# Performance work log

Hardware: AMD Instinct MI355X
Metric: run time of the kernel (lower is better)

Reference implementation:

```python
import jax, jax.numpy as jnp
import numpy as np

LN_EPS = 1e-5


def setup_inputs() -> dict:
    key = jax.random.key(0)
    ks = jax.random.split(key, 5)
    N, E, D = 50000, 600000, 128
    x = jax.random.normal(ks[0], (N, D), dtype=jnp.float32)
    edge_index = jax.random.randint(ks[1], (2, E), 0, N, dtype=jnp.int64)
    W_l = jax.random.normal(ks[2], (D, D), dtype=jnp.float32) * (1.0 / np.sqrt(D))
    b_l = jnp.zeros((D,), dtype=jnp.float32)
    W_r = jax.random.normal(ks[3], (D, D), dtype=jnp.float32) * (1.0 / np.sqrt(D))
    gamma = jnp.ones((D,), dtype=jnp.float32)
    beta = jnp.zeros((D,), dtype=jnp.float32)
    return {"x": x, "edge_index": edge_index, "W_l": W_l, "b_l": b_l,
            "W_r": W_r, "gamma": gamma, "beta": beta}


def reference(x, edge_index, W_l, b_l, W_r, gamma, beta):
    # SAGEConv (mean aggregation): out = lin_l(mean_{j in N(i)} x_j) + lin_r(x_i)
    N = x.shape[0]
    src, dst = edge_index[0], edge_index[1]
    msg = x[src]                                                # (E, D) gather
    agg = jax.ops.segment_sum(msg, dst, num_segments=N)         # (N, D) scatter-add
    cnt = jax.ops.segment_sum(jnp.ones_like(dst, dtype=x.dtype), dst, num_segments=N)
    mean = agg / jnp.maximum(cnt, 1.0)[:, None]
    h = mean @ W_l.T + b_l + x @ W_r.T                          # (N, D)
    # LayerNorm over feature dim
    mu = jnp.mean(h, axis=-1, keepdims=True)
    var = jnp.mean(jnp.square(h - mu), axis=-1, keepdims=True)
    h = (h - mu) * jax.lax.rsqrt(var + LN_EPS) * gamma + beta
    # ReLU; Dropout is identity in eval mode
    return jax.nn.relu(h)
```

## Files before the change

kernel.cpp:

```cpp
#include <hip/hip_runtime.h>
#include <stdint.h>

#define DIM 128
#define LN_EPS 1e-5f
#define BROWS 32
#define BINB 128
#define SCAP 16
#define NBKT_MAX 1600
#define LELLS 56
#define LOVF 64
#define OVFCAP 4096
#define ATS 264
#define PINIT ((int)0xAAAAAAAA)

typedef __attribute__((ext_vector_type(8))) short bf16x8;
typedef __attribute__((ext_vector_type(4))) float f32x4;

static __device__ __forceinline__ uint16_t f2bf(float f) {
    uint32_t u = __float_as_uint(f);
    return (uint16_t)((u + 0x7fffu + ((u >> 16) & 1u)) >> 16);
}
static __device__ __forceinline__ float bf_lo(uint32_t w) {
    return __uint_as_float(w << 16);
}
static __device__ __forceinline__ float bf_hi(uint32_t w) {
    return __uint_as_float(w & 0xffff0000u);
}

__global__ __launch_bounds__(256) void bin_kernel(
    const int* __restrict__ ei,
    const float* __restrict__ x,
    const float* __restrict__ Wl,
    const float* __restrict__ Wr,
    int* __restrict__ cnt, uint32_t* __restrict__ bedge,
    int* __restrict__ novf, int* __restrict__ ovf,
    uint16_t* __restrict__ x16, uint16_t* __restrict__ wc,
    int E, int N, int nbkt)
{
    __shared__ int hist[NBKT_MAX];
    const int t = threadIdx.x, b = blockIdx.x;

    for (int i = t; i < nbkt; i += 256) hist[i] = 0;
    __syncthreads();

    const int chunk = (E + BINB - 1) / BINB;
    const int e0 = b * chunk;
    const int e1 = (e0 + chunk < E) ? e0 + chunk : E;

    for (int e = e0 + t; e < e1; e += 256)
        atomicAdd(&hist[ei[E + e] >> 5], 1);
    __syncthreads();

    for (int i = t; i < nbkt; i += 256) {
        cnt[(size_t)i * BINB + b] = hist[i];
        hist[i] = 0;
    }
    __syncthreads();

    for (int e = e0 + t; e < e1; e += 256) {
        int src = ei[e];
        int dst = ei[E + e];
        int bkt = dst >> 5;
        int r = atomicAdd(&hist[bkt], 1);
        if (r < SCAP) {
            bedge[((size_t)bkt * BINB + b) * SCAP + r] =
                ((uint32_t)(dst & 31) << 27) | (uint32_t)src;
        } else {
            int q = atomicAdd(novf, 1) - PINIT;
            if (q >= 0 && q < OVFCAP) { ovf[2 * q] = dst; ovf[2 * q + 1] = src; }
        }
    }

    {
        int tid = b * 256 + t, nth = BINB * 256;
        int nxp = (N * DIM) >> 1;
        for (int i = tid; i < nxp; i += nth) {
            float2 v = *(const float2*)(x + 2 * i);
            uint32_t u = ((uint32_t)f2bf(v.y) << 16) | (uint32_t)f2bf(v.x);
            ((uint32_t*)x16)[i] = u;
        }
        for (int i = tid; i < DIM * 256; i += nth) {
            int d = i >> 8, k = i & 255;
            float v = (k < DIM) ? Wl[d * DIM + k] : Wr[d * DIM + (k - DIM)];
            wc[i] = f2bf(v);
        }
    }
}

__global__ __launch_bounds__(256, 4) void fused_kernel(
    const uint16_t* __restrict__ x16,
    const int* __restrict__ cnt,
    const uint32_t* __restrict__ bedge,
    const int* __restrict__ novf,
    const int* __restrict__ ovf,
    const uint16_t* __restrict__ wc,
    const float* __restrict__ bl,
    const float* __restrict__ gma,
    const float* __restrict__ bta,
    float* __restrict__ out,
    int N, int E)
{
    __shared__ int ell_s[BROWS][LELLS];
    __shared__ int cnt_s[BROWS];
    __shared__ int lovf_s[LOVF];
    __shared__ int nlovf_s;
    __shared__ uint16_t atile[2][16 * ATS];
    __shared__ float pln[2][16][2][2];

    const int t    = threadIdx.x;
    const int lane = t & 63;
    const int w    = t >> 6;
    const int p    = w >> 1;
    const int h    = w & 1;
    const int tile_row0 = blockIdx.x * BROWS + p * 16;
    const int grow0     = tile_row0 + h * 8;
    const int lb        = p * 16 + h * 8;

    if (t < BROWS) cnt_s[t] = 0;
    if (t == BROWS) nlovf_s = 0;
    __syncthreads();

    if (t < BINB) {
        int c = cnt[(size_t)blockIdx.x * BINB + t];
        c = (c < SCAP) ? c : SCAP;
        const uint32_t* sp = bedge + ((size_t)blockIdx.x * BINB + t) * SCAP;
        for (int r = 0; r < c; ++r) {
            uint32_t pk = sp[r];
            int local = pk >> 27;
            int rr = atomicAdd(&cnt_s[local], 1);
            if (rr < LELLS) ell_s[local][rr] = (int)(pk & 0x07FFFFFF);
            else {
                int q = atomicAdd(&nlovf_s, 1);
                if (q < LOVF) lovf_s[q] = (int)pk;
            }
        }
    }
    __syncthreads();

    int dgx[8], nell[8], mx = 0;
    #pragma unroll
    for (int r = 0; r < 8; ++r) {
        int d = __builtin_amdgcn_readfirstlane(cnt_s[lb + r]);
        dgx[r] = d;
        int tt = d < LELLS ? d : LELLS;
        nell[r] = tt;
        mx = (tt > mx) ? tt : mx;
    }

    int sidx[8];
    #pragma unroll
    for (int r = 0; r < 8; ++r)
        sidx[r] = (lane < nell[r]) ? ell_s[lb + r][lane] : 0;

    float m0[8], m1[8];
    #pragma unroll
    for (int r = 0; r < 8; ++r) { m0[r] = 0.0f; m1[r] = 0.0f; }

    for (int j = 0; j < mx; ++j) {
        #pragma unroll
        for (int r = 0; r < 8; ++r) {
            float pr = (j < nell[r]) ? 1.0f : 0.0f;
            int s = __builtin_amdgcn_readlane(sidx[r], j);
            uint32_t u = *(const uint32_t*)(x16 + (size_t)s * DIM + 2 * lane);
            m0[r] = fmaf(pr, bf_lo(u), m0[r]);
            m1[r] = fmaf(pr, bf_hi(u), m1[r]);
        }
    }

    {
        int nl = __builtin_amdgcn_readfirstlane(nlovf_s);
        nl = (nl < 0) ? 0 : (nl > LOVF ? LOVF : nl);
        for (int i = 0; i < nl; ++i) {
            uint32_t pk = (uint32_t)lovf_s[i];
            int local = pk >> 27;
            if (local >= lb && local < lb + 8) {
                int srco = (int)(pk & 0x07FFFFFF);
                uint32_t u = *(const uint32_t*)(x16 + (size_t)srco * DIM + 2 * lane);
                float v0 = bf_lo(u), v1 = bf_hi(u);
                #pragma unroll
                for (int r = 0; r < 8; ++r) {
                    float pr = (local == lb + r) ? 1.0f : 0.0f;
                    m0[r] = fmaf(pr, v0, m0[r]);
                    m1[r] = fmaf(pr, v1, m1[r]);
                }
            }
        }
    }

    {
        int no = __builtin_amdgcn_readfirstlane(novf[0]) - PINIT;
        no = (no < 0) ? 0 : (no > OVFCAP ? OVFCAP : no);
        for (int i = 0; i < no; ++i) {
            int dsto = __builtin_amdgcn_readfirstlane(ovf[2 * i]);
            int srco = __builtin_amdgcn_readfirstlane(ovf[2 * i + 1]);
            if (dsto >= grow0 && dsto < grow0 + 8) {
                uint32_t u = *(const uint32_t*)(x16 + (size_t)srco * DIM + 2 * lane);
                float v0 = bf_lo(u), v1 = bf_hi(u);
                #pragma unroll
                for (int r = 0; r < 8; ++r) {
                    bool hit = (dsto == grow0 + r);
                    float pr = hit ? 1.0f : 0.0f;
                    m0[r] = fmaf(pr, v0, m0[r]);
                    m1[r] = fmaf(pr, v1, m1[r]);
                    dgx[r] += hit ? 1 : 0;
                }
            }
        }
    }

    {
        uint16_t* at = atile[p];
        #pragma unroll
        for (int r = 0; r < 8; ++r) {
            int row = grow0 + r;
            int rr = (row < N) ? row : 0;
            float rc = (dgx[r] > 0) ? (1.0f / (float)dgx[r]) : 0.0f;
            int lr = h * 8 + r;
            ushort2 mu2;
            mu2.x = f2bf(m0[r] * rc);
            mu2.y = f2bf(m1[r] * rc);
            *(ushort2*)&at[lr * ATS + 2 * lane] = mu2;
            uint32_t xv = *(const uint32_t*)(x16 + (size_t)rr * DIM + 2 * lane);
            *(uint32_t*)&at[lr * ATS + 128 + 2 * lane] = xv;
        }
    }
    __syncthreads();

    const int nsub = lane & 15;
    const int quad = lane >> 4;
    const uint16_t* at = atile[p];

    f32x4 acc[4];
    #pragma unroll
    for (int tt = 0; tt < 4; ++tt) {
        float b = bl[(h * 4 + tt) * 16 + nsub];
        acc[tt] = (f32x4){b, b, b, b};
    }

    #pragma unroll
    for (int c = 0; c < 8; ++c) {
        bf16x8 af = *(const bf16x8*)&at[nsub * ATS + c * 32 + quad * 8];
        #pragma unroll
        for (int tt = 0; tt < 4; ++tt) {
            int tg = h * 4 + tt;
            bf16x8 bfr = *(const bf16x8*)&wc[(size_t)(tg * 16 + nsub) * 256 + c * 32 + quad * 8];
            acc[tt] = __builtin_amdgcn_mfma_f32_16x16x32_bf16(af, bfr, acc[tt], 0, 0, 0);
        }
    }

    #pragma unroll
    for (int i = 0; i < 4; ++i) {
        float s = 0.0f, q = 0.0f;
        #pragma unroll
        for (int tt = 0; tt < 4; ++tt) {
            float v = acc[tt][i];
            s += v;
            q += v * v;
        }
        #pragma unroll
        for (int off = 1; off < 16; off <<= 1) {
            s += __shfl_xor(s, off, 64);
            q += __shfl_xor(q, off, 64);
        }
        if (nsub == 0) {
            pln[p][quad * 4 + i][h][0] = s;
            pln[p][quad * 4 + i][h][1] = q;
        }
    }
    __syncthreads();

    #pragma unroll
    for (int i = 0; i < 4; ++i) {
        int lrow = quad * 4 + i;
        float s = pln[p][lrow][0][0] + pln[p][lrow][1][0];
        float q = pln[p][lrow][0][1] + pln[p][lrow][1][1];
        float mu = s * (1.0f / 128.0f);
        float var = q * (1.0f / 128.0f) - mu * mu;
        float rs = rsqrtf(fmaxf(var, 0.0f) + LN_EPS);
        int grow = tile_row0 + lrow;
        if (grow < N) {
            float* op = out + (size_t)grow * DIM;
            #pragma unroll
            for (int tt = 0; tt < 4; ++tt) {
                int f = (h * 4 + tt) * 16 + nsub;
                float o = fmaxf((acc[tt][i] - mu) * rs * gma[f] + bta[f], 0.0f);
                op[f] = o;
            }
        }
    }
}

extern "C" void kernel_launch(void* const* d_in, const int* in_sizes, int n_in,
                              void* d_out, int out_size, void* d_ws, size_t ws_size,
                              hipStream_t stream) {
    const float* x  = (const float*)d_in[0];
    const int* ei   = (const int*)d_in[1];
    const float* Wl = (const float*)d_in[2];
    const float* bl = (const float*)d_in[3];
    const float* Wr = (const float*)d_in[4];
    const float* ga = (const float*)d_in[5];
    const float* be = (const float*)d_in[6];
    float* out = (float*)d_out;

    int N = in_sizes[0] / DIM;
    int E = in_sizes[1] / 2;
    int nbkt = (N + BROWS - 1) / BROWS;

    int* cnt        = (int*)d_ws;
    int* novf       = cnt + (size_t)nbkt * BINB;
    uint16_t* wc    = (uint16_t*)(novf + 16);
    uint16_t* x16   = wc + DIM * 256;
    uint32_t* bedge = (uint32_t*)(x16 + (size_t)N * DIM);
    int* ovf        = (int*)(bedge + (size_t)nbkt * BINB * SCAP);

    bin_kernel<<<BINB, 256, 0, stream>>>(
        ei, x, Wl, Wr, cnt, bedge, novf, ovf, x16, wc, E, N, nbkt);

    fused_kernel<<<nbkt, 256, 0, stream>>>(
        x16, cnt, bedge, novf, ovf, wc, bl, ga, be, out, N, E);
}
```

Measured before the change: 187.5 us.

## Widen binning kernel, shrink count bytes, and software-pipeline neighbor gathers

The binning kernel now runs 256 blocks of 1024 threads with a per-slot capacity of 8, and per-block bucket counts are stored as saturated bytes instead of ints, so the count array that the fused kernel reads shrinks. In the fused kernel, the neighbor gather loop prefetches the next iteration's eight rows while accumulating the current ones, and source indices are pre-shifted to byte offsets. This aims to hide gather latency and cut binning and count traffic. In exchange it raises register pressure, and the smaller slot capacity can push more edges into the shared overflow path.

```diff
diff --git a/kernel.cpp b/kernel.cpp
--- a/kernel.cpp
+++ b/kernel.cpp
@@ -4,8 +4,9 @@
 #define DIM 128
 #define LN_EPS 1e-5f
 #define BROWS 32
-#define BINB 128
-#define SCAP 16
+#define BINB 256
+#define NT1 1024
+#define SCAP 8
 #define NBKT_MAX 1600
 #define LELLS 56
 #define LOVF 64
@@ -27,12 +28,12 @@
     return __uint_as_float(w & 0xffff0000u);
 }
 
-__global__ __launch_bounds__(256) void bin_kernel(
+__global__ __launch_bounds__(NT1) void bin_kernel(
     const int* __restrict__ ei,
     const float* __restrict__ x,
     const float* __restrict__ Wl,
     const float* __restrict__ Wr,
-    int* __restrict__ cnt, uint32_t* __restrict__ bedge,
+    uint8_t* __restrict__ cnt, uint32_t* __restrict__ bedge,
     int* __restrict__ novf, int* __restrict__ ovf,
     uint16_t* __restrict__ x16, uint16_t* __restrict__ wc,
     int E, int N, int nbkt)
@@ -40,24 +41,25 @@
     __shared__ int hist[NBKT_MAX];
     const int t = threadIdx.x, b = blockIdx.x;
 
-    for (int i = t; i < nbkt; i += 256) hist[i] = 0;
+    for (int i = t; i < nbkt; i += NT1) hist[i] = 0;
     __syncthreads();
 
     const int chunk = (E + BINB - 1) / BINB;
     const int e0 = b * chunk;
     const int e1 = (e0 + chunk < E) ? e0 + chunk : E;
 
-    for (int e = e0 + t; e < e1; e += 256)
+    for (int e = e0 + t; e < e1; e += NT1)
         atomicAdd(&hist[ei[E + e] >> 5], 1);
     __syncthreads();
 
-    for (int i = t; i < nbkt; i += 256) {
-        cnt[(size_t)i * BINB + b] = hist[i];
+    for (int i = t; i < nbkt; i += NT1) {
+        int c = hist[i];
+        cnt[(size_t)i * BINB + b] = (uint8_t)(c > 255 ? 255 : c);
         hist[i] = 0;
     }
     __syncthreads();
 
-    for (int e = e0 + t; e < e1; e += 256) {
+    for (int e = e0 + t; e < e1; e += NT1) {
         int src = ei[e];
         int dst = ei[E + e];
         int bkt = dst >> 5;
@@ -72,7 +74,7 @@
     }
 
     {
-        int tid = b * 256 + t, nth = BINB * 256;
+        int tid = b * NT1 + t, nth = BINB * NT1;
         int nxp = (N * DIM) >> 1;
         for (int i = tid; i < nxp; i += nth) {
             float2 v = *(const float2*)(x + 2 * i);
@@ -89,7 +91,7 @@
 
 __global__ __launch_bounds__(256, 4) void fused_kernel(
     const uint16_t* __restrict__ x16,
-    const int* __restrict__ cnt,
+    const uint8_t* __restrict__ cnt,
     const uint32_t* __restrict__ bedge,
     const int* __restrict__ novf,
     const int* __restrict__ ovf,
@@ -147,23 +149,37 @@
         mx = (tt > mx) ? tt : mx;
     }
 
-    int sidx[8];
+    int soff[8];
     #pragma unroll
     for (int r = 0; r < 8; ++r)
-        sidx[r] = (lane < nell[r]) ? ell_s[lb + r][lane] : 0;
+        soff[r] = (lane < nell[r]) ? (ell_s[lb + r][lane] << 8) : 0;
 
     float m0[8], m1[8];
     #pragma unroll
     for (int r = 0; r < 8; ++r) { m0[r] = 0.0f; m1[r] = 0.0f; }
 
+    const char* xb = (const char*)x16;
+    uint32_t u[8];
+    #pragma unroll
+    for (int r = 0; r < 8; ++r) {
+        int o = __builtin_amdgcn_readlane(soff[r], 0);
+        u[r] = *(const uint32_t*)(xb + (uint32_t)o + 4 * lane);
+    }
+
     for (int j = 0; j < mx; ++j) {
+        uint32_t un[8];
+        int jn = (j + 1 < mx) ? j + 1 : j;
+        #pragma unroll
+        for (int r = 0; r < 8; ++r) {
+            int o = __builtin_amdgcn_readlane(soff[r], jn);
+            un[r] = *(const uint32_t*)(xb + (uint32_t)o + 4 * lane);
+        }
         #pragma unroll
         for (int r = 0; r < 8; ++r) {
             float pr = (j < nell[r]) ? 1.0f : 0.0f;
-            int s = __builtin_amdgcn_readlane(sidx[r], j);
-            uint32_t u = *(const uint32_t*)(x16 + (size_t)s * DIM + 2 * lane);
-            m0[r] = fmaf(pr, bf_lo(u), m0[r]);
-            m1[r] = fmaf(pr, bf_hi(u), m1[r]);
+            m0[r] = fmaf(pr, bf_lo(u[r]), m0[r]);
+            m1[r] = fmaf(pr, bf_hi(u[r]), m1[r]);
+            u[r] = un[r];
         }
     }
 
@@ -175,8 +191,8 @@
             int local = pk >> 27;
             if (local >= lb && local < lb + 8) {
                 int srco = (int)(pk & 0x07FFFFFF);
-                uint32_t u = *(const uint32_t*)(x16 + (size_t)srco * DIM + 2 * lane);
-                float v0 = bf_lo(u), v1 = bf_hi(u);
+                uint32_t uu = *(const uint32_t*)(x16 + (size_t)srco * DIM + 2 * lane);
+                float v0 = bf_lo(uu), v1 = bf_hi(uu);
                 #pragma unroll
                 for (int r = 0; r < 8; ++r) {
                     float pr = (local == lb + r) ? 1.0f : 0.0f;
@@ -194,8 +210,8 @@
             int dsto = __builtin_amdgcn_readfirstlane(ovf[2 * i]);
             int srco = __builtin_amdgcn_readfirstlane(ovf[2 * i + 1]);
             if (dsto >= grow0 && dsto < grow0 + 8) {
-                uint32_t u = *(const uint32_t*)(x16 + (size_t)srco * DIM + 2 * lane);
-                float v0 = bf_lo(u), v1 = bf_hi(u);
+                uint32_t uu = *(const uint32_t*)(x16 + (size_t)srco * DIM + 2 * lane);
+                float v0 = bf_lo(uu), v1 = bf_hi(uu);
                 #pragma unroll
                 for (int r = 0; r < 8; ++r) {
                     bool hit = (dsto == grow0 + r);
@@ -306,14 +322,14 @@
     int E = in_sizes[1] / 2;
     int nbkt = (N + BROWS - 1) / BROWS;
 
-    int* cnt        = (int*)d_ws;
-    int* novf       = cnt + (size_t)nbkt * BINB;
+    uint8_t* cnt    = (uint8_t*)d_ws;
+    int* novf       = (int*)(cnt + (size_t)nbkt * BINB);
     uint16_t* wc    = (uint16_t*)(novf + 16);
     uint16_t* x16   = wc + DIM * 256;
     uint32_t* bedge = (uint32_t*)(x16 + (size_t)N * DIM);
     int* ovf        = (int*)(bedge + (size_t)nbkt * BINB * SCAP);
 
-    bin_kernel<<<BINB, 256, 0, stream>>>(
+    bin_kernel<<<BINB, NT1, 0, stream>>>(
         ei, x, Wl, Wr, cnt, bedge, novf, ovf, x16, wc, E, N, nbkt);
 
     fused_kernel<<<nbkt, 256, 0, stream>>>(
```

Measured after the change: 168.0 us. -10.4%, faster.
